# Kernel tuning notes

Measured on AMD Instinct MI355X. Metric: run time of the kernel, lower is better.

The kernel has to match this reference:

```python
import jax, jax.numpy as jnp
import numpy as np

BLOCK = 32      # config.BLOCK_SIZE
PSF_WN = 64     # config.PSF_WINDOW_N (upsampled block size == PSF kernel size)
DX = 1e-06      # config.PIX_SIZE


def images_to_blocks(imgs, B):
    # Faithful to torch reshape/permute chain: block order is (nBW outer, nBH inner)
    N, H, W = imgs.shape
    nBH, nBW = H // B, W // B
    x = imgs.reshape(N, nBH, B, nBW, B)
    x = jnp.transpose(x, (0, 2, 4, 3, 1))        # [N,B,B,nBW,nBH]
    x = x.reshape(N, B, B, nBW * nBH)
    return jnp.transpose(x, (0, 3, 1, 2))        # [N,P,B,B]


def upsample_nearest(blocks, U):
    # torch F.interpolate(mode='nearest'): src index = floor(dst * B / U)
    N, P, B, _ = blocks.shape
    idx = (jnp.arange(U) * B) // U
    return blocks[:, :, idx[:, None], idx[None, :]]  # [N,P,U,U]


def depthwise_full_conv(x, w):
    # per-region cross-correlation with padding K-1 ("full"), groups=P
    N, P, K, _ = x.shape
    return jax.lax.conv_general_dilated(
        x, w[:, None, :, :], window_strides=(1, 1),
        padding=[(K - 1, K - 1), (K - 1, K - 1)],
        dimension_numbers=('NCHW', 'OIHW', 'NCHW'),
        feature_group_count=P)                   # [N,P,2K-1,2K-1]


def splat_blocks_to_sensor(block_out, x_centers, y_centers, X_N, Y_N, dx):
    # Vectorized scatter-add replacing the per-region python loop; out-of-bounds dropped
    N, P, Hk, Wk = block_out.shape
    hk = Hk // 2
    cx, cy = X_N // 2, Y_N // 2
    ic = cx + jnp.round(x_centers / dx).astype(jnp.int32)   # [P]
    jc = cy + jnp.round(y_centers / dx).astype(jnp.int32)
    I = ic[:, None] - hk + jnp.arange(Hk)                   # [P,Hk]
    J = jc[:, None] - hk + jnp.arange(Wk)                   # [P,Wk]
    lin = I[:, :, None] * Y_N + J[:, None, :]               # [P,Hk,Wk]
    ok = ((I >= 0) & (I < X_N))[:, :, None] & ((J >= 0) & (J < Y_N))[:, None, :]
    lin = jnp.where(ok, lin, -1).reshape(-1)
    sensor = jnp.zeros((N, X_N * Y_N), block_out.dtype)
    sensor = sensor.at[:, lin].add(block_out.reshape(N, -1), mode='drop')
    return sensor.reshape(N, X_N, Y_N)


def setup_inputs() -> dict:
    key = jax.random.key(0)
    k1, k2 = jax.random.split(key)
    N, H, W = 8, 512, 512
    P = (H // BLOCK) * (W // BLOCK)   # 256
    X_N = Y_N = 1024
    imgs = jax.random.uniform(k1, (N, H, W), jnp.float32)
    psf_stack = jax.random.uniform(k2, (P, PSF_WN, PSF_WN), jnp.float32)
    psf_stack = psf_stack / jnp.sum(psf_stack, axis=(1, 2), keepdims=True)
    # 16x16 grid of physical region centers, 48-pixel pitch (integer pixels so round() is exact)
    grid = jnp.arange(P)
    rows = (grid % 16).astype(jnp.float32)
    cols = (grid // 16).astype(jnp.float32)
    x_centers = (rows - 7.0) * 48.0 * DX
    y_centers = (cols - 7.0) * 48.0 * DX
    Xg, Yg = jnp.meshgrid(jnp.arange(X_N, dtype=jnp.float32) * DX,
                          jnp.arange(Y_N, dtype=jnp.float32) * DX, indexing='ij')
    return {"imgs": imgs, "psf_stack": psf_stack, "X": Xg, "Y": Yg,
            "x_centers": x_centers, "y_centers": y_centers}


def reference(imgs, psf_stack, X, Y, x_centers, y_centers):
    blocks = images_to_blocks(imgs, BLOCK)               # [N,P,32,32]
    blocks_up = upsample_nearest(blocks, PSF_WN)         # [N,P,64,64]
    block_out = depthwise_full_conv(blocks_up, psf_stack)  # [N,P,127,127]
    X_N, Y_N = X.shape
    return splat_blocks_to_sensor(block_out, x_centers, y_centers, X_N, Y_N, DX)
```

## Files before the change

kernel.cpp:

```cpp
#include <hip/hip_runtime.h>

typedef _Float16 h8 __attribute__((ext_vector_type(8)));
typedef float    f4 __attribute__((ext_vector_type(4)));
typedef unsigned int u4 __attribute__((ext_vector_type(4)));

#define IMG_N 8
#define IMG_H 512
#define IMG_W 512
#define P_CNT 256
#define PSFN  64
#define SENS  1024
#define TILE_FLOATS 16256

#define KT_HALVES (4*33*2*104)
#define BT_COLS   97
#define BT_HALVES (BT_COLS*40)

__global__ __launch_bounds__(256, 2) void svconv_main(
    const float* __restrict__ imgs, const float* __restrict__ psf,
    float* __restrict__ ws)
{
    __shared__ float ps[PSFN * PSFN];
    __shared__ __align__(16) _Float16 Kt[KT_HALVES];
    __shared__ __align__(16) _Float16 BT[BT_HALVES];

    const int bid = blockIdx.x;
    const int n = bid >> 8, p = bid & 255;
    const int bh = p & 15, bw = p >> 4;
    const int tid = threadIdx.x;
    const int wv = tid >> 6, lane = tid & 63;
    const int m = lane & 15, q = lane >> 4;

    {
        const float4* pp = (const float4*)(psf + (size_t)p * PSFN * PSFN);
        float4* pd = (float4*)ps;
        for (int i = tid; i < PSFN * PSFN / 4; i += 256) pd[i] = pp[i];
        const u4 z = {0u, 0u, 0u, 0u};
        u4* kz = (u4*)Kt;
        for (int i = tid; i < KT_HALVES / 8; i += 256) kz[i] = z;
        for (int i = tid; i < BT_HALVES; i += 256) BT[i] = (_Float16)0.f;
    }
    __syncthreads();

    for (int idx = tid; idx < 4 * 33 * 33; idx += 256) {
        const int e = idx % 33;
        const int gc = idx / 33;
        const int g = gc % 33;
        const int cls = gc / 33;
        const int pi = cls >> 1, pj = cls & 1;
        const int E = pi ? 32 : 33;
        if (e < E) {
            const int a = 2 * e - 1 + pi;
            const int b = 2 * g - 1 + pj;
            float sv = 0.f;
            #pragma unroll
            for (int du = 0; du < 2; ++du) {
                const int x = a + du;
                if ((unsigned)x < 64u) {
                    #pragma unroll
                    for (int dv = 0; dv < 2; ++dv) {
                        const int y = b + dv;
                        if ((unsigned)y < 64u) sv += ps[x * 64 + y];
                    }
                }
            }
            const _Float16 hv = (_Float16)sv;
            const int base = (cls * 33 + g) * 208;
            const int t = e + 32;
            Kt[base + t]           = hv;
            Kt[base + 104 + t - 1] = hv;
        }
    }
    {
        const int r0 = tid >> 5, c = tid & 31;
        const float* src = imgs + ((size_t)n * IMG_H + bh * 32) * IMG_W + bw * 32;
        for (int r = r0; r < 32; r += 8)
            BT[(c + 32) * 40 + r] = (_Float16)src[r * IMG_W + c];
    }
    __syncthreads();

    const int cls = wv, pi = cls >> 1, pj = cls & 1;
    const int U0 = pi ? 31 : 32;
    const char* ktc = (const char*)Kt;
    const char* btc = (const char*)BT + pj * 80;

    int aoff[4];
    #pragma unroll
    for (int ut = 0; ut < 4; ++ut) {
        const int t0 = 8 * q - m + (U0 - 16 * ut) + 32;
        const int s  = t0 & 1;
        aoff[ut] = (cls * 33) * 416 + s * 208 + (t0 - s) * 2;
    }
    int boff[4];
    #pragma unroll
    for (int vt = 0; vt < 4; ++vt) boff[vt] = (16 * vt + m) * 80 + q * 16;

    f4 acc[4][4];
    #pragma unroll
    for (int ut = 0; ut < 4; ++ut)
        #pragma unroll
        for (int vt = 0; vt < 4; ++vt) acc[ut][vt] = (f4){0.f, 0.f, 0.f, 0.f};

    #pragma unroll 1
    for (int g = 0; g < 33; ++g) {
        h8 B[4];
        #pragma unroll
        for (int vt = 0; vt < 4; ++vt)
            B[vt] = *(const h8*)(btc + boff[vt] + g * 80);
        h8 A[4];
        #pragma unroll
        for (int ut = 0; ut < 4; ++ut) {
            const unsigned* ap = (const unsigned*)(ktc + aoff[ut] + g * 416);
            u4 d = {ap[0], ap[1], ap[2], ap[3]};
            A[ut] = __builtin_bit_cast(h8, d);
        }
        #pragma unroll
        for (int ut = 0; ut < 4; ++ut)
            #pragma unroll
            for (int vt = 0; vt < 4; ++vt)
                acc[ut][vt] = __builtin_amdgcn_mfma_f32_16x16x32_f16(
                    A[ut], B[vt], acc[ut][vt], 0, 0, 0);
    }

    float* tile = ws + (size_t)(n * P_CNT + p) * TILE_FLOATS;
    const int plane = pi ? (8192 + pj * 4032) : (pj * 4096);
    #pragma unroll
    for (int ut = 0; ut < 4; ++ut) {
        #pragma unroll
        for (int reg = 0; reg < 4; ++reg) {
            const int u = 16 * ut + 4 * q + reg;
            if (pi == 0 || u < 63) {
                float* rp = tile + plane + u * 64 + m;
                #pragma unroll
                for (int vt = 0; vt < 4; ++vt) rp[16 * vt] = acc[ut][vt][reg];
            }
        }
    }
}

__global__ __launch_bounds__(256) void svconv_gather(
    const float* __restrict__ ws, float* __restrict__ out)
{
    const int b = blockIdx.x;
    const int n = b >> 10, x = b & 1023;
    int bhlo = (x + 288) / 48 - 10; if (bhlo < 0) bhlo = 0;
    int bhhi = (x < 113) ? -1 : ((x - 113) / 48);
    if (bhhi > 15) bhhi = 15;
    const float* wsn = ws + (size_t)n * P_CNT * TILE_FLOATS;
    float* outrow = out + ((size_t)n << 20) + (size_t)x * SENS;

    for (int yb = 0; yb < 4; ++yb) {
        const int y = yb * 256 + threadIdx.x;
        int bwlo = (y + 288) / 48 - 10; if (bwlo < 0) bwlo = 0;
        int bwhi = (y < 113) ? -1 : ((y - 113) / 48);
        if (bwhi > 15) bwhi = 15;
        float s = 0.0f;
        for (int bhh = bhlo; bhh <= bhhi; ++bhh) {
            const int ti = x - 113 - 48 * bhh;
            const int pi = ti & 1, uu = ti >> 1;
            for (int bww = bwlo; bww <= bwhi; ++bww) {
                const int tj = y - 113 - 48 * bww;
                const int pj = tj & 1, vv = tj >> 1;
                const int base = pi ? (8192 + pj * 4032) : (pj * 4096);
                s += wsn[(size_t)(bww * 16 + bhh) * TILE_FLOATS + base + uu * 64 + vv];
            }
        }
        outrow[y] = s;
    }
}

extern "C" void kernel_launch(void* const* d_in, const int* in_sizes, int n_in,
                              void* d_out, int out_size, void* d_ws, size_t ws_size,
                              hipStream_t stream) {
    const float* imgs = (const float*)d_in[0];
    const float* psf  = (const float*)d_in[1];
    float* out = (float*)d_out;
    float* ws  = (float*)d_ws;

    svconv_main<<<dim3(IMG_N * P_CNT), dim3(256), 0, stream>>>(imgs, psf, ws);
    svconv_gather<<<dim3(IMG_N * SENS), dim3(256), 0, stream>>>(ws, out);
}
```

Measured before the change: 215.5 us.

## Precompute PSF MFMA fragments once per region and store intermediate tiles in fp16

Adds a prep kernel that builds the polyphase PSF A-fragments once per region (256 blocks) into global memory, instead of every one of the 2048 main blocks rebuilding them in shared memory. The main kernel now loads A fragments directly from global/L2, uses less LDS, and raises occupancy to 4 blocks per CU. Intermediate tiles are written and read as fp16 instead of fp32, halving workspace traffic between the main and gather kernels. The risks are an extra launch, global-memory latency for A loads, and lower precision in the accumulated output.

```diff
diff --git a/kernel.cpp b/kernel.cpp
--- a/kernel.cpp
+++ b/kernel.cpp
@@ -10,49 +10,35 @@
 #define P_CNT 256
 #define PSFN  64
 #define SENS  1024
-#define TILE_FLOATS 16256
-
-#define KT_HALVES (4*33*2*104)
+
+#define TILE_HALVES 16256
+#define TILES_BYTES ((size_t)IMG_N * P_CNT * TILE_HALVES * 2)
+
+#define KW     90
+#define KFRAG_PER_P (4 * 33 * KW)
+
 #define BT_COLS   97
-#define BT_HALVES (BT_COLS*40)
-
-__global__ __launch_bounds__(256, 2) void svconv_main(
-    const float* __restrict__ imgs, const float* __restrict__ psf,
-    float* __restrict__ ws)
+#define BT_HALVES (BT_COLS * 40)
+
+__global__ __launch_bounds__(256) void svconv_prep(
+    const float* __restrict__ psf, u4* __restrict__ kfrag)
 {
     __shared__ float ps[PSFN * PSFN];
-    __shared__ __align__(16) _Float16 Kt[KT_HALVES];
-    __shared__ __align__(16) _Float16 BT[BT_HALVES];
-
-    const int bid = blockIdx.x;
-    const int n = bid >> 8, p = bid & 255;
-    const int bh = p & 15, bw = p >> 4;
-    const int tid = threadIdx.x;
-    const int wv = tid >> 6, lane = tid & 63;
-    const int m = lane & 15, q = lane >> 4;
-
-    {
-        const float4* pp = (const float4*)(psf + (size_t)p * PSFN * PSFN);
-        float4* pd = (float4*)ps;
-        for (int i = tid; i < PSFN * PSFN / 4; i += 256) pd[i] = pp[i];
-        const u4 z = {0u, 0u, 0u, 0u};
-        u4* kz = (u4*)Kt;
-        for (int i = tid; i < KT_HALVES / 8; i += 256) kz[i] = z;
-        for (int i = tid; i < BT_HALVES; i += 256) BT[i] = (_Float16)0.f;
-    }
+    __shared__ float Kc[4 * 33 * 33];
+    const int p = blockIdx.x, tid = threadIdx.x;
+
+    const float4* pp = (const float4*)(psf + (size_t)p * PSFN * PSFN);
+    float4* pd = (float4*)ps;
+    for (int i = tid; i < PSFN * PSFN / 4; i += 256) pd[i] = pp[i];
     __syncthreads();
 
     for (int idx = tid; idx < 4 * 33 * 33; idx += 256) {
-        const int e = idx % 33;
-        const int gc = idx / 33;
-        const int g = gc % 33;
-        const int cls = gc / 33;
+        const int g = idx % 33, e = (idx / 33) % 33, cls = idx / 1089;
         const int pi = cls >> 1, pj = cls & 1;
         const int E = pi ? 32 : 33;
+        float sv = 0.f;
         if (e < E) {
-            const int a = 2 * e - 1 + pi;
-            const int b = 2 * g - 1 + pj;
-            float sv = 0.f;
+            const int a = 2 * e - 1 + pi, b = 2 * g - 1 + pj;
             #pragma unroll
             for (int du = 0; du < 2; ++du) {
                 const int x = a + du;
@@ -64,13 +50,42 @@
                     }
                 }
             }
-            const _Float16 hv = (_Float16)sv;
-            const int base = (cls * 33 + g) * 208;
-            const int t = e + 32;
-            Kt[base + t]           = hv;
-            Kt[base + 104 + t - 1] = hv;
-        }
-    }
+        }
+        Kc[idx] = sv;
+    }
+    __syncthreads();
+
+    u4* kout = kfrag + (size_t)p * KFRAG_PER_P;
+    for (int idx = tid; idx < KFRAG_PER_P; idx += 256) {
+        const int w = idx % KW;
+        const int g = (idx / KW) % 33;
+        const int cls = idx / (KW * 33);
+        h8 hv;
+        #pragma unroll
+        for (int j = 0; j < 8; ++j) {
+            const int e = w + j - 32;
+            const float v = ((unsigned)e < 33u) ? Kc[cls * 1089 + e * 33 + g] : 0.f;
+            hv[j] = (_Float16)v;
+        }
+        kout[idx] = __builtin_bit_cast(u4, hv);
+    }
+}
+
+__global__ __launch_bounds__(256, 4) void svconv_main(
+    const float* __restrict__ imgs, const u4* __restrict__ kfrag,
+    _Float16* __restrict__ tiles)
+{
+    __shared__ __align__(16) _Float16 BT[BT_HALVES];
+
+    const int bid = blockIdx.x;
+    const int n = bid >> 8, p = bid & 255;
+    const int bh = p & 15, bw = p >> 4;
+    const int tid = threadIdx.x;
+    const int wv = tid >> 6, lane = tid & 63;
+    const int m = lane & 15, q = lane >> 4;
+
+    for (int i = tid; i < BT_HALVES; i += 256) BT[i] = (_Float16)0.f;
+    __syncthreads();
     {
         const int r0 = tid >> 5, c = tid & 31;
         const float* src = imgs + ((size_t)n * IMG_H + bh * 32) * IMG_W + bw * 32;
@@ -81,39 +96,39 @@
 
     const int cls = wv, pi = cls >> 1, pj = cls & 1;
     const int U0 = pi ? 31 : 32;
-    const char* ktc = (const char*)Kt;
     const char* btc = (const char*)BT + pj * 80;
 
-    int aoff[4];
-    #pragma unroll
-    for (int ut = 0; ut < 4; ++ut) {
-        const int t0 = 8 * q - m + (U0 - 16 * ut) + 32;
-        const int s  = t0 & 1;
-        aoff[ut] = (cls * 33) * 416 + s * 208 + (t0 - s) * 2;
-    }
     int boff[4];
     #pragma unroll
     for (int vt = 0; vt < 4; ++vt) boff[vt] = (16 * vt + m) * 80 + q * 16;
 
+    const char* ka[4];
+    {
+        const char* base = (const char*)(kfrag + (size_t)p * KFRAG_PER_P
+                                         + cls * 33 * KW);
+        #pragma unroll
+        for (int ut = 0; ut < 4; ++ut) {
+            const int t0 = 8 * q - m + (U0 - 16 * ut) + 32;
+            ka[ut] = base + t0 * 16;
+        }
+    }
+
     f4 acc[4][4];
     #pragma unroll
     for (int ut = 0; ut < 4; ++ut)
         #pragma unroll
         for (int vt = 0; vt < 4; ++vt) acc[ut][vt] = (f4){0.f, 0.f, 0.f, 0.f};
 
-    #pragma unroll 1
+    #pragma unroll 3
     for (int g = 0; g < 33; ++g) {
+        h8 A[4];
+        #pragma unroll
+        for (int ut = 0; ut < 4; ++ut)
+            A[ut] = __builtin_bit_cast(h8, *(const u4*)(ka[ut] + g * (KW * 16)));
         h8 B[4];
         #pragma unroll
         for (int vt = 0; vt < 4; ++vt)
             B[vt] = *(const h8*)(btc + boff[vt] + g * 80);
-        h8 A[4];
-        #pragma unroll
-        for (int ut = 0; ut < 4; ++ut) {
-            const unsigned* ap = (const unsigned*)(ktc + aoff[ut] + g * 416);
-            u4 d = {ap[0], ap[1], ap[2], ap[3]};
-            A[ut] = __builtin_bit_cast(h8, d);
-        }
         #pragma unroll
         for (int ut = 0; ut < 4; ++ut)
             #pragma unroll
@@ -122,7 +137,7 @@
                     A[ut], B[vt], acc[ut][vt], 0, 0, 0);
     }
 
-    float* tile = ws + (size_t)(n * P_CNT + p) * TILE_FLOATS;
+    _Float16* tile = tiles + (size_t)(n * P_CNT + p) * TILE_HALVES;
     const int plane = pi ? (8192 + pj * 4032) : (pj * 4096);
     #pragma unroll
     for (int ut = 0; ut < 4; ++ut) {
@@ -130,23 +145,24 @@
         for (int reg = 0; reg < 4; ++reg) {
             const int u = 16 * ut + 4 * q + reg;
             if (pi == 0 || u < 63) {
-                float* rp = tile + plane + u * 64 + m;
+                _Float16* rp = tile + plane + u * 64 + m;
                 #pragma unroll
-                for (int vt = 0; vt < 4; ++vt) rp[16 * vt] = acc[ut][vt][reg];
+                for (int vt = 0; vt < 4; ++vt)
+                    rp[16 * vt] = (_Float16)acc[ut][vt][reg];
             }
         }
     }
 }
 
 __global__ __launch_bounds__(256) void svconv_gather(
-    const float* __restrict__ ws, float* __restrict__ out)
+    const _Float16* __restrict__ ws, float* __restrict__ out)
 {
     const int b = blockIdx.x;
     const int n = b >> 10, x = b & 1023;
     int bhlo = (x + 288) / 48 - 10; if (bhlo < 0) bhlo = 0;
     int bhhi = (x < 113) ? -1 : ((x - 113) / 48);
     if (bhhi > 15) bhhi = 15;
-    const float* wsn = ws + (size_t)n * P_CNT * TILE_FLOATS;
+    const _Float16* wsn = ws + (size_t)n * P_CNT * TILE_HALVES;
     float* outrow = out + ((size_t)n << 20) + (size_t)x * SENS;
 
     for (int yb = 0; yb < 4; ++yb) {
@@ -162,7 +178,8 @@
                 const int tj = y - 113 - 48 * bww;
                 const int pj = tj & 1, vv = tj >> 1;
                 const int base = pi ? (8192 + pj * 4032) : (pj * 4096);
-                s += wsn[(size_t)(bww * 16 + bhh) * TILE_FLOATS + base + uu * 64 + vv];
+                s += (float)wsn[(size_t)(bww * 16 + bhh) * TILE_HALVES
+                                + base + uu * 64 + vv];
             }
         }
         outrow[y] = s;
@@ -175,8 +192,10 @@
     const float* imgs = (const float*)d_in[0];
     const float* psf  = (const float*)d_in[1];
     float* out = (float*)d_out;
-    float* ws  = (float*)d_ws;
-
-    svconv_main<<<dim3(IMG_N * P_CNT), dim3(256), 0, stream>>>(imgs, psf, ws);
-    svconv_gather<<<dim3(IMG_N * SENS), dim3(256), 0, stream>>>(ws, out);
-}
+    _Float16* tiles = (_Float16*)d_ws;
+    u4* kfrag = (u4*)((char*)d_ws + TILES_BYTES);
+
+    svconv_prep<<<dim3(P_CNT), dim3(256), 0, stream>>>(psf, kfrag);
+    svconv_main<<<dim3(IMG_N * P_CNT), dim3(256), 0, stream>>>(imgs, kfrag, tiles);
+    svconv_gather<<<dim3(IMG_N * SENS), dim3(256), 0, stream>>>(tiles, out);
+}
```

Measured after the change: 228.3 us. 1.06x slower.
